# Performance work log

Hardware: AMD Instinct MI355X
Metric: run time of the kernel (lower is better)

The kernel has to match this reference:

```python
import jax, jax.numpy as jnp
import numpy as np

H, L, D, R = 16, 4096, 64, 128   # heads, seq len, head dim, FAVOR+ feature dim
S_SCALE = 0.125                  # attention inner-product scaling S
CHUNK = 128                      # chunk size for causal linear attention
EPS = 1e-10                      # module's self.epsilon denominator guard


def _get_proj(d, r, seed=0):
    # get_proj(R, D, orthogonal=True, hyperbolic=True): QR-orthogonalized
    # Gaussian block rescaled by chi column norms, then [W, -W].
    rng = np.random.RandomState(seed)
    rh = r // 2
    w = rng.randn(d, rh)
    chis = np.linalg.norm(w, ord=2, axis=0, keepdims=True)
    qm, _ = np.linalg.qr(w, mode='reduced')
    w = qm * chis
    return np.concatenate((w, -w), axis=1).astype(np.float32)  # (D, R)


def setup_inputs() -> dict:
    key = jax.random.key(0)
    kq, kk, kv = jax.random.split(key, 3)
    q = jax.random.normal(kq, (H, L, D), dtype=jnp.float32)
    k = jax.random.normal(kk, (H, L, D), dtype=jnp.float32)
    v = jax.random.normal(kv, (H, L, D), dtype=jnp.float32)
    W = jnp.asarray(_get_proj(D, R))
    return {"T": 64, "k": k, "q": q, "v": v, "W": W}


def _phi(x, W):
    # FAVOR+ feature map: x' = x * S^0.5 / D^0.25;
    # phi(x) = exp(W^T x' - ||x'||^2 / 2) / sqrt(R)
    xs = x * (S_SCALE ** 0.5 / D ** 0.25)            # (H, L, D)
    Wx = jnp.einsum('hld,dr->hlr', xs, W)            # (H, L, R)
    sq = 0.5 * jnp.sum(xs * xs, axis=-1, keepdims=True)
    return jnp.exp(Wx - sq) / (R ** 0.5)             # (H, L, R)


def reference(T, k, q, v, W):
    # Deterministic FAVOR+ estimator of the strictly-causal softmax attention
    # Pred_l = sum_{j<l} v_j exp(S<q_l,k_j>) / sum_{i<l} exp(S<q_l,k_i>)
    # which the tree+sampling machinery approximates (T = sampling budget,
    # irrelevant for the exact kernel estimate). Chunked linear attention.
    del T
    pq = _phi(q, W)                                  # (H, L, R)
    pk = _phi(k, W)                                  # (H, L, R)
    nc = L // CHUNK
    pq_c = pq.reshape(H, nc, CHUNK, R)
    pk_c = pk.reshape(H, nc, CHUNK, R)
    v_c = v.reshape(H, nc, CHUNK, D)
    # per-chunk KV summaries and exclusive prefix over chunks
    skv = jnp.einsum('hncr,hncd->hnrd', pk_c, v_c)   # (H, nc, R, D)
    zk = jnp.sum(pk_c, axis=2)                       # (H, nc, R)
    skv_prev = jnp.cumsum(skv, axis=1) - skv         # exclusive
    zk_prev = jnp.cumsum(zk, axis=1) - zk
    num_inter = jnp.einsum('hncr,hnrd->hncd', pq_c, skv_prev)
    den_inter = jnp.einsum('hncr,hnr->hnc', pq_c, zk_prev)
    # intra-chunk strictly-causal part (j < l)
    A = jnp.einsum('hncr,hnsr->hncs', pq_c, pk_c)    # (H, nc, C, C)
    mask = jnp.tril(jnp.ones((CHUNK, CHUNK), dtype=A.dtype), k=-1)
    A = A * mask
    num_intra = jnp.einsum('hncs,hnsd->hncd', A, v_c)
    den_intra = jnp.sum(A, axis=-1)
    out = (num_inter + num_intra) / (den_inter + den_intra + EPS)[..., None]
    return out.reshape(H, L, D)
```

## Files before the change

### kernel.cpp

```cpp
#include <hip/hip_runtime.h>

#define H 16
#define L 4096
#define D 64
#define R 128
#define C2 64
#define NC2 64
#define HN2 (H * NC2)
#define EPS 1e-10f
#define XS_SCALE 0.125f
#define PHI_SCALE 0.08838834764831845f

typedef __attribute__((ext_vector_type(8))) short bf8;
typedef __attribute__((ext_vector_type(4))) short bf4;
typedef __attribute__((ext_vector_type(16))) float facc16;

static __device__ __forceinline__ unsigned short f2b(float f) {
    unsigned u = __float_as_uint(f);
    return (unsigned short)((u + 0x7fffu + ((u >> 16) & 1u)) >> 16);
}
static __device__ __forceinline__ float b2f(unsigned short s) {
    return __uint_as_float(((unsigned)s) << 16);
}

__global__ __launch_bounds__(256) void kW(const float* __restrict__ W,
                                          unsigned short* __restrict__ Wtg) {
    for (int i = threadIdx.x; i < 8192; i += 256) {
        int d = i >> 7, r = i & 127;
        Wtg[(unsigned)((r * 64 + d) ^ ((r & 7) << 3))] = f2b(W[i]);
    }
}

__global__ __launch_bounds__(256, 4) void k1(
    const float* __restrict__ q, const float* __restrict__ k,
    const float* __restrict__ v, const unsigned short* __restrict__ Wtg,
    unsigned short* __restrict__ pq, unsigned short* __restrict__ pk,
    unsigned short* __restrict__ vTg, unsigned short* __restrict__ skvTp,
    float* __restrict__ zk)
{
    __shared__ __align__(16) unsigned short A_[8192];
    __shared__ __align__(16) unsigned short B_[4096];
    __shared__ __align__(16) unsigned short C_[8192];
    const int tid = threadIdx.x, hn = blockIdx.x;
    const int lane = tid & 63, wave = tid >> 6, lo = lane & 31, hi = lane >> 5;
    const int rg = wave & 1, ch = wave >> 1;
    const size_t cbase = (size_t)hn * C2 * D;
    const int prow = tid >> 4, pd0 = (tid & 15) * 4;

    float4 kv4[4];
    #pragma unroll
    for (int n = 0; n < 4; ++n)
        kv4[n] = *(const float4*)(k + cbase + (prow + 16 * n) * 64 + pd0);
    for (int i = tid; i < 1024; i += 256)
        *(bf8*)&A_[i * 8] = *(const bf8*)(Wtg + i * 8);
    #pragma unroll
    for (int n = 0; n < 4; ++n) {
        int row = prow + 16 * n;
        float4 vv = *(const float4*)(q + cbase + row * 64 + pd0);
        unsigned* p = (unsigned*)&B_[(unsigned)((row * 64 + pd0) ^ ((row & 7) << 3))];
        p[0] = (unsigned)f2b(vv.x * XS_SCALE) | ((unsigned)f2b(vv.y * XS_SCALE) << 16);
        p[1] = (unsigned)f2b(vv.z * XS_SCALE) | ((unsigned)f2b(vv.w * XS_SCALE) << 16);
    }
    __syncthreads();

    {
        bf8 af[4]; float ssq = 0.f;
        #pragma unroll
        for (int s = 0; s < 4; ++s) {
            af[s] = *(const bf8*)&B_[(unsigned)(((rg * 32 + lo) * 64 + 16 * s + 8 * hi) ^ ((lo & 7) << 3))];
            #pragma unroll
            for (int e = 0; e < 8; ++e) { float t = b2f((unsigned short)af[s][e]); ssq += t * t; }
        }
        ssq += __shfl_xor(ssq, 32); ssq *= 0.5f;
        float sqrow[16];
        #pragma unroll
        for (int reg = 0; reg < 16; ++reg)
            sqrow[reg] = __shfl(ssq, (reg & 3) + 8 * (reg >> 2) + 4 * hi);
        facc16 acc[2];
        #pragma unroll
        for (int t = 0; t < 2; ++t)
            #pragma unroll
            for (int e = 0; e < 16; ++e) acc[t][e] = 0.f;
        #pragma unroll
        for (int s = 0; s < 4; ++s)
            #pragma unroll
            for (int t = 0; t < 2; ++t) {
                const bf8 b = *(const bf8*)&A_[(unsigned)((((2 * ch + t) * 32 + lo) * 64 + 16 * s + 8 * hi) ^ ((lo & 7) << 3))];
                acc[t] = __builtin_amdgcn_mfma_f32_32x32x16_bf16(af[s], b, acc[t], 0, 0, 0);
            }
        #pragma unroll
        for (int t = 0; t < 2; ++t)
            #pragma unroll
            for (int reg = 0; reg < 16; ++reg) {
                int row = rg * 32 + (reg & 3) + 8 * (reg >> 2) + 4 * hi;
                int col = (2 * ch + t) * 32 + lo;
                C_[(unsigned)((row * 128 + col) ^ ((row & 15) << 3))] =
                    f2b(__expf(acc[t][reg] - sqrow[reg]) * PHI_SCALE);
            }
    }
    __syncthreads();

    float4 vv4[4];
    #pragma unroll
    for (int n = 0; n < 4; ++n)
        vv4[n] = *(const float4*)(v + cbase + (prow + 16 * n) * 64 + pd0);
    for (int i = tid; i < 1024; i += 256)
        *(bf8*)(pq + (size_t)hn * 8192 + i * 8) = *(const bf8*)&C_[i * 8];
    #pragma unroll
    for (int n = 0; n < 4; ++n) {
        int row = prow + 16 * n;
        unsigned* p = (unsigned*)&B_[(unsigned)((row * 64 + pd0) ^ ((row & 7) << 3))];
        p[0] = (unsigned)f2b(kv4[n].x * XS_SCALE) | ((unsigned)f2b(kv4[n].y * XS_SCALE) << 16);
        p[1] = (unsigned)f2b(kv4[n].z * XS_SCALE) | ((unsigned)f2b(kv4[n].w * XS_SCALE) << 16);
    }
    __syncthreads();

    facc16 acck[2];
    float sqk[16];
    {
        bf8 af[4]; float ssq = 0.f;
        #pragma unroll
        for (int s = 0; s < 4; ++s) {
            af[s] = *(const bf8*)&B_[(unsigned)(((rg * 32 + lo) * 64 + 16 * s + 8 * hi) ^ ((lo & 7) << 3))];
            #pragma unroll
            for (int e = 0; e < 8; ++e) { float t = b2f((unsigned short)af[s][e]); ssq += t * t; }
        }
        ssq += __shfl_xor(ssq, 32); ssq *= 0.5f;
        #pragma unroll
        for (int reg = 0; reg < 16; ++reg)
            sqk[reg] = __shfl(ssq, (reg & 3) + 8 * (reg >> 2) + 4 * hi);
        #pragma unroll
        for (int t = 0; t < 2; ++t)
            #pragma unroll
            for (int e = 0; e < 16; ++e) acck[t][e] = 0.f;
        #pragma unroll
        for (int s = 0; s < 4; ++s)
            #pragma unroll
            for (int t = 0; t < 2; ++t) {
                const bf8 b = *(const bf8*)&A_[(unsigned)((((2 * ch + t) * 32 + lo) * 64 + 16 * s + 8 * hi) ^ ((lo & 7) << 3))];
                acck[t] = __builtin_amdgcn_mfma_f32_32x32x16_bf16(af[s], b, acck[t], 0, 0, 0);
            }
    }
    __syncthreads();

    #pragma unroll
    for (int t = 0; t < 2; ++t) {
        int colr = (2 * ch + t) * 32 + lo;
        #pragma unroll
        for (int g = 0; g < 4; ++g) {
            int c0 = rg * 32 + 8 * g + 4 * hi;
            bf4 pk4;
            #pragma unroll
            for (int e = 0; e < 4; ++e) {
                unsigned short b = f2b(__expf(acck[t][4 * g + e] - sqk[4 * g + e]) * PHI_SCALE);
                pk4[e] = (short)b;
                C_[(unsigned)(((c0 + e) * 128 + colr) ^ (((c0 + e) & 15) << 3))] = b;
            }
            *(bf4*)&A_[(unsigned)((colr * 64 + c0) ^ ((colr & 7) << 3))] = pk4;
        }
    }
    #pragma unroll
    for (int n = 0; n < 4; ++n) {
        int row = prow + 16 * n;
        unsigned* p = (unsigned*)&B_[(unsigned)((row * 64 + pd0) ^ ((row & 7) << 3))];
        p[0] = (unsigned)f2b(vv4[n].x) | ((unsigned)f2b(vv4[n].y) << 16);
        p[1] = (unsigned)f2b(vv4[n].z) | ((unsigned)f2b(vv4[n].w) << 16);
    }
    __syncthreads();

    for (int i = tid; i < 1024; i += 256)
        *(bf8*)(pk + (size_t)hn * 8192 + i * 8) = *(const bf8*)&C_[i * 8];
    if (tid < 128) {
        float s = 0.f;
        #pragma unroll
        for (int j = 0; j < 8; ++j) {
            bf8 a8 = *(const bf8*)&A_[(unsigned)((tid * 64 + 8 * j) ^ ((tid & 7) << 3))];
            #pragma unroll
            for (int e = 0; e < 8; ++e) s += b2f((unsigned short)a8[e]);
        }
        zk[(size_t)hn * 128 + tid] = s;
    }
    bf8 aid[2];
    #pragma unroll
    for (int s2 = 0; s2 < 2; ++s2)
        #pragma unroll
        for (int e = 0; e < 8; ++e)
            aid[s2][e] = (e == lo - 16 * s2 - 8 * hi) ? (short)0x3F80 : (short)0;
    facc16 tv[2][2];
    #pragma unroll
    for (int t = 0; t < 2; ++t)
        #pragma unroll
        for (int u = 0; u < 2; ++u) {
            #pragma unroll
            for (int e = 0; e < 16; ++e) tv[t][u][e] = 0.f;
            #pragma unroll
            for (int s2 = 0; s2 < 2; ++s2) {
                const bf8 b = *(const bf8*)&B_[(unsigned)(((32 * u + lo) * 64 + 16 * (2 * t + s2) + 8 * hi) ^ ((lo & 7) << 3))];
                tv[t][u] = __builtin_amdgcn_mfma_f32_32x32x16_bf16(aid[s2], b, tv[t][u], 0, 0, 0);
            }
        }
    __syncthreads();

    #pragma unroll
    for (int t = 0; t < 2; ++t)
        #pragma unroll
        for (int u = 0; u < 2; ++u)
            #pragma unroll
            for (int reg = 0; reg < 16; ++reg) {
                int d = 32 * t + (reg & 3) + 8 * (reg >> 2) + 4 * hi;
                int c = 32 * u + lo;
                C_[(unsigned)((d * 64 + c) ^ ((d & 7) << 3))] = f2b(tv[t][u][reg]);
            }
    __syncthreads();

    for (int i = tid; i < 512; i += 256)
        *(bf8*)(vTg + (size_t)hn * 4096 + i * 8) = *(const bf8*)&C_[i * 8];
    {
        facc16 acs[2];
        #pragma unroll
        for (int t = 0; t < 2; ++t)
            #pragma unroll
            for (int e = 0; e < 16; ++e) acs[t][e] = 0.f;
        #pragma unroll
        for (int s = 0; s < 4; ++s) {
            const bf8 a = *(const bf8*)&C_[(unsigned)(((rg * 32 + lo) * 64 + 16 * s + 8 * hi) ^ ((lo & 7) << 3))];
            #pragma unroll
            for (int t = 0; t < 2; ++t) {
                const bf8 b = *(const bf8*)&A_[(unsigned)((((2 * ch + t) * 32 + lo) * 64 + 16 * s + 8 * hi) ^ ((lo & 7) << 3))];
                acs[t] = __builtin_amdgcn_mfma_f32_32x32x16_bf16(a, b, acs[t], 0, 0, 0);
            }
        }
        unsigned short* sg = skvTp + (size_t)hn * 8192;
        #pragma unroll
        for (int t = 0; t < 2; ++t)
            #pragma unroll
            for (int reg = 0; reg < 16; ++reg) {
                int d = rg * 32 + (reg & 3) + 8 * (reg >> 2) + 4 * hi;
                int r = (2 * ch + t) * 32 + lo;
                sg[d * 128 + r] = f2b(acs[t][reg]);
            }
    }
}

__global__ __launch_bounds__(256) void k2(unsigned short* __restrict__ skvTp,
                                          const float* __restrict__ zk,
                                          unsigned short* __restrict__ zkp)
{
    const int bid = blockIdx.x, tid = threadIdx.x;
    if (bid < 512) {
        int g = bid * 256 + tid;
        int h = g >> 13, dr = g & 8191;
        unsigned short* p = skvTp + (size_t)h * NC2 * 8192 + dr;
        unsigned short vals[NC2];
        #pragma unroll
        for (int n = 0; n < NC2; ++n) vals[n] = p[(size_t)n * 8192];
        float run = 0.f;
        #pragma unroll
        for (int n = 0; n < NC2; ++n) {
            float t = b2f(vals[n]);
            p[(size_t)n * 8192] = f2b(run);
            run += t;
        }
    } else {
        int g2 = (bid - 512) * 256 + tid;
        int h = g2 >> 7, r = g2 & 127;
        const float* pz = zk + (size_t)h * NC2 * 128 + r;
        unsigned short* oz = zkp + (size_t)h * NC2 * 128 + r;
        float vals[NC2];
        #pragma unroll
        for (int n = 0; n < NC2; ++n) vals[n] = pz[n * 128];
        float run = 0.f;
        #pragma unroll
        for (int n = 0; n < NC2; ++n) {
            oz[n * 128] = f2b(run);
            run += vals[n];
        }
    }
}

__global__ __launch_bounds__(256) void k3(
    const unsigned short* __restrict__ pq, const unsigned short* __restrict__ pk,
    const unsigned short* __restrict__ vTg, const unsigned short* __restrict__ skvTp,
    const unsigned short* __restrict__ zkp, float* __restrict__ out)
{
    __shared__ __align__(16) unsigned short P_[8192];
    __shared__ __align__(16) unsigned short Q_[8192];
    __shared__ __align__(16) unsigned short V_[4096];
    const int tid = threadIdx.x, hn = blockIdx.x;
    const int lane = tid & 63, wave = tid >> 6, lo = lane & 31, hi = lane >> 5;
    const int rg = wave & 1, ch = wave >> 1;

    for (int i = tid; i < 1024; i += 256)
        *(bf8*)&P_[i * 8] = *(const bf8*)(pq + (size_t)hn * 8192 + i * 8);
    for (int i = tid; i < 1024; i += 256)
        *(bf8*)&Q_[i * 8] = *(const bf8*)(pk + (size_t)hn * 8192 + i * 8);
    for (int i = tid; i < 512; i += 256)
        *(bf8*)&V_[i * 8] = *(const bf8*)(vTg + (size_t)hn * 4096 + i * 8);
    __syncthreads();

    bf8 qf[8];
    #pragma unroll
    for (int s = 0; s < 8; ++s)
        qf[s] = *(const bf8*)&P_[(unsigned)(((rg * 32 + lo) * 128 + 16 * s + 8 * hi) ^ ((lo & 15) << 3))];
    __syncthreads();

    for (int i = tid; i < 1024; i += 256) {
        bf8 t8 = *(const bf8*)(skvTp + (size_t)hn * 8192 + i * 8);
        int d = i >> 4, r0 = (i & 15) * 8;
        *(bf8*)&P_[(unsigned)((d * 128 + r0) ^ ((d & 15) << 3))] = t8;
    }
    bf8 onesf, zf[8];
    #pragma unroll
    for (int e = 0; e < 8; ++e) onesf[e] = (lo == 0) ? (short)0x3F80 : (short)0;
    #pragma unroll
    for (int s = 0; s < 8; ++s)
        #pragma unroll
        for (int e = 0; e < 8; ++e) zf[s][e] = 0;
    if (lo == 0) {
        #pragma unroll
        for (int s = 0; s < 8; ++s)
            zf[s] = *(const bf8*)(zkp + (size_t)hn * 128 + 16 * s + 8 * hi);
    }

    facc16 ac1;
    #pragma unroll
    for (int e = 0; e < 16; ++e) ac1[e] = 0.f;
    #pragma unroll
    for (int s = 0; s < 8; ++s) {
        const bf8 b = *(const bf8*)&Q_[(unsigned)(((ch * 32 + lo) * 128 + 16 * s + 8 * hi) ^ ((lo & 15) << 3))];
        ac1 = __builtin_amdgcn_mfma_f32_32x32x16_bf16(qf[s], b, ac1, 0, 0, 0);
    }
    __syncthreads();

    #pragma unroll
    for (int reg = 0; reg < 16; ++reg) {
        int row = rg * 32 + (reg & 3) + 8 * (reg >> 2) + 4 * hi;
        int sc = ch * 32 + lo;
        Q_[(unsigned)((row * 64 + sc) ^ ((row & 7) << 3))] = f2b(sc < row ? ac1[reg] : 0.f);
    }
    __syncthreads();

    facc16 an, ad;
    #pragma unroll
    for (int e = 0; e < 16; ++e) { an[e] = 0.f; ad[e] = 0.f; }
    #pragma unroll
    for (int s = 0; s < 4; ++s) {
        const bf8 a = *(const bf8*)&Q_[(unsigned)(((rg * 32 + lo) * 64 + 16 * s + 8 * hi) ^ ((lo & 7) << 3))];
        const bf8 b = *(const bf8*)&V_[(unsigned)(((ch * 32 + lo) * 64 + 16 * s + 8 * hi) ^ ((lo & 7) << 3))];
        an = __builtin_amdgcn_mfma_f32_32x32x16_bf16(a, b, an, 0, 0, 0);
        ad = __builtin_amdgcn_mfma_f32_32x32x16_bf16(a, onesf, ad, 0, 0, 0);
    }
    #pragma unroll
    for (int s = 0; s < 8; ++s) {
        const bf8 b = *(const bf8*)&P_[(unsigned)(((ch * 32 + lo) * 128 + 16 * s + 8 * hi) ^ ((lo & 15) << 3))];
        an = __builtin_amdgcn_mfma_f32_32x32x16_bf16(qf[s], b, an, 0, 0, 0);
        ad = __builtin_amdgcn_mfma_f32_32x32x16_bf16(qf[s], zf[s], ad, 0, 0, 0);
    }
    float* og = out + (size_t)hn * C2 * D;
    #pragma unroll
    for (int reg = 0; reg < 16; ++reg) {
        int row = rg * 32 + (reg & 3) + 8 * (reg >> 2) + 4 * hi;
        float dv = __shfl(ad[reg], lane & 32);
        og[row * 64 + ch * 32 + lo] = an[reg] / (dv + EPS);
    }
}

extern "C" void kernel_launch(void* const* d_in, const int* in_sizes, int n_in,
                              void* d_out, int out_size, void* d_ws, size_t ws_size,
                              hipStream_t stream) {
    const float* k = (const float*)d_in[1];
    const float* q = (const float*)d_in[2];
    const float* v = (const float*)d_in[3];
    const float* W = (const float*)d_in[4];
    float* out = (float*)d_out;

    unsigned short* pq    = (unsigned short*)d_ws;
    unsigned short* pk    = pq + (size_t)HN2 * 8192;
    unsigned short* vTg   = pk + (size_t)HN2 * 8192;
    unsigned short* skvTp = vTg + (size_t)HN2 * 4096;
    unsigned short* Wtg   = skvTp + (size_t)HN2 * 8192;
    unsigned short* zkp   = Wtg + 8192;
    float* zk             = (float*)(zkp + (size_t)HN2 * 128);

    kW<<<1, 256, 0, stream>>>(W, Wtg);
    k1<<<HN2, 256, 0, stream>>>(q, k, v, Wtg, pq, pk, vTg, skvTp, zk);
    k2<<<520, 256, 0, stream>>>(skvTp, zk, zkp);
    k3<<<HN2, 256, 0, stream>>>(pq, pk, vTg, skvTp, zkp, out);
}
```

Measured before the change: 63.44 us.

## Store intermediates in MFMA fragment order and load operands directly from global

Stores W, phi(q), phi(k) and v^T in global memory already laid out as per-lane MFMA fragments. The consumer kernels can then load operands straight from global memory instead of staging them through LDS with barriers. k1 now reads q and k directly into registers and computes the squared norm in fp32. The zk column sum becomes an MFMA against a ones vector, and f2b switches to the HIP bf16 intrinsic. This cuts LDS traffic and barriers, and frees LDS in k3 for occupancy, at the cost of more scattered global loads that lean on the cache.

```diff
diff --git a/kernel.cpp b/kernel.cpp
--- a/kernel.cpp
+++ b/kernel.cpp
@@ -1,4 +1,5 @@
 #include <hip/hip_runtime.h>
+#include <hip/hip_bf16.h>
 
 #define H 16
 #define L 4096
@@ -16,26 +17,33 @@
 typedef __attribute__((ext_vector_type(16))) float facc16;
 
 static __device__ __forceinline__ unsigned short f2b(float f) {
-    unsigned u = __float_as_uint(f);
-    return (unsigned short)((u + 0x7fffu + ((u >> 16) & 1u)) >> 16);
+    union { __hip_bfloat16 h; unsigned short u; } c;
+    c.h = __float2bfloat16(f);
+    return c.u;
 }
 static __device__ __forceinline__ float b2f(unsigned short s) {
     return __uint_as_float(((unsigned)s) << 16);
 }
 
 __global__ __launch_bounds__(256) void kW(const float* __restrict__ W,
-                                          unsigned short* __restrict__ Wtg) {
-    for (int i = threadIdx.x; i < 8192; i += 256) {
-        int d = i >> 7, r = i & 127;
-        Wtg[(unsigned)((r * 64 + d) ^ ((r & 7) << 3))] = f2b(W[i]);
+                                          unsigned short* __restrict__ WF) {
+    __shared__ float wl[8192];
+    for (int i = threadIdx.x; i < 8192; i += 256) wl[i] = W[i];
+    __syncthreads();
+    for (int i = threadIdx.x; i < 1024; i += 256) {
+        int tile = i >> 8, s = (i >> 6) & 3, hi = (i >> 5) & 1, lo = i & 31;
+        int r = tile * 32 + lo;
+        #pragma unroll
+        for (int e = 0; e < 8; ++e)
+            WF[i * 8 + e] = f2b(wl[(16 * s + 8 * hi + e) * 128 + r]);
     }
 }
 
 __global__ __launch_bounds__(256, 4) void k1(
     const float* __restrict__ q, const float* __restrict__ k,
-    const float* __restrict__ v, const unsigned short* __restrict__ Wtg,
-    unsigned short* __restrict__ pq, unsigned short* __restrict__ pk,
-    unsigned short* __restrict__ vTg, unsigned short* __restrict__ skvTp,
+    const float* __restrict__ v, const unsigned short* __restrict__ WF,
+    unsigned short* __restrict__ pqF, unsigned short* __restrict__ pkF,
+    unsigned short* __restrict__ vTF, unsigned short* __restrict__ skvTp,
     float* __restrict__ zk)
 {
     __shared__ __align__(16) unsigned short A_[8192];
@@ -47,35 +55,29 @@
     const size_t cbase = (size_t)hn * C2 * D;
     const int prow = tid >> 4, pd0 = (tid & 15) * 4;
 
-    float4 kv4[4];
-    #pragma unroll
-    for (int n = 0; n < 4; ++n)
-        kv4[n] = *(const float4*)(k + cbase + (prow + 16 * n) * 64 + pd0);
-    for (int i = tid; i < 1024; i += 256)
-        *(bf8*)&A_[i * 8] = *(const bf8*)(Wtg + i * 8);
-    #pragma unroll
-    for (int n = 0; n < 4; ++n) {
-        int row = prow + 16 * n;
-        float4 vv = *(const float4*)(q + cbase + row * 64 + pd0);
-        unsigned* p = (unsigned*)&B_[(unsigned)((row * 64 + pd0) ^ ((row & 7) << 3))];
-        p[0] = (unsigned)f2b(vv.x * XS_SCALE) | ((unsigned)f2b(vv.y * XS_SCALE) << 16);
-        p[1] = (unsigned)f2b(vv.z * XS_SCALE) | ((unsigned)f2b(vv.w * XS_SCALE) << 16);
-    }
-    __syncthreads();
-
-    {
-        bf8 af[4]; float ssq = 0.f;
+    bf8 af[4];
+    float sqrow[16];
+    {
+        float ssq = 0.f;
         #pragma unroll
         for (int s = 0; s < 4; ++s) {
-            af[s] = *(const bf8*)&B_[(unsigned)(((rg * 32 + lo) * 64 + 16 * s + 8 * hi) ^ ((lo & 7) << 3))];
-            #pragma unroll
-            for (int e = 0; e < 8; ++e) { float t = b2f((unsigned short)af[s][e]); ssq += t * t; }
+            const float* qp = q + cbase + (rg * 32 + lo) * 64 + 16 * s + 8 * hi;
+            float4 f0 = *(const float4*)qp;
+            float4 f1 = *(const float4*)(qp + 4);
+            float x0 = f0.x * XS_SCALE, x1 = f0.y * XS_SCALE, x2 = f0.z * XS_SCALE, x3 = f0.w * XS_SCALE;
+            float x4 = f1.x * XS_SCALE, x5 = f1.y * XS_SCALE, x6 = f1.z * XS_SCALE, x7 = f1.w * XS_SCALE;
+            ssq += x0*x0 + x1*x1 + x2*x2 + x3*x3 + x4*x4 + x5*x5 + x6*x6 + x7*x7;
+            bf8 a;
+            a[0]=(short)f2b(x0); a[1]=(short)f2b(x1); a[2]=(short)f2b(x2); a[3]=(short)f2b(x3);
+            a[4]=(short)f2b(x4); a[5]=(short)f2b(x5); a[6]=(short)f2b(x6); a[7]=(short)f2b(x7);
+            af[s] = a;
         }
         ssq += __shfl_xor(ssq, 32); ssq *= 0.5f;
-        float sqrow[16];
-        #pragma unroll
-        for (int reg = 0; reg < 16; ++reg)
-            sqrow[reg] = __shfl(ssq, (reg & 3) + 8 * (reg >> 2) + 4 * hi);
+        #pragma unroll
+        for (int r2 = 0; r2 < 16; ++r2)
+            sqrow[r2] = __shfl(ssq, (r2 & 3) + 8 * (r2 >> 2) + 4 * hi);
+    }
+    {
         facc16 acc[2];
         #pragma unroll
         for (int t = 0; t < 2; ++t)
@@ -85,7 +87,7 @@
         for (int s = 0; s < 4; ++s)
             #pragma unroll
             for (int t = 0; t < 2; ++t) {
-                const bf8 b = *(const bf8*)&A_[(unsigned)((((2 * ch + t) * 32 + lo) * 64 + 16 * s + 8 * hi) ^ ((lo & 7) << 3))];
+                const bf8 b = *(const bf8*)(WF + (((2 * ch + t) * 4 + s) * 64 + hi * 32 + lo) * 8);
                 acc[t] = __builtin_amdgcn_mfma_f32_32x32x16_bf16(af[s], b, acc[t], 0, 0, 0);
             }
         #pragma unroll
@@ -100,47 +102,48 @@
     }
     __syncthreads();
 
-    float4 vv4[4];
-    #pragma unroll
-    for (int n = 0; n < 4; ++n)
-        vv4[n] = *(const float4*)(v + cbase + (prow + 16 * n) * 64 + pd0);
-    for (int i = tid; i < 1024; i += 256)
-        *(bf8*)(pq + (size_t)hn * 8192 + i * 8) = *(const bf8*)&C_[i * 8];
-    #pragma unroll
-    for (int n = 0; n < 4; ++n) {
-        int row = prow + 16 * n;
-        unsigned* p = (unsigned*)&B_[(unsigned)((row * 64 + pd0) ^ ((row & 7) << 3))];
-        p[0] = (unsigned)f2b(kv4[n].x * XS_SCALE) | ((unsigned)f2b(kv4[n].y * XS_SCALE) << 16);
-        p[1] = (unsigned)f2b(kv4[n].z * XS_SCALE) | ((unsigned)f2b(kv4[n].w * XS_SCALE) << 16);
-    }
-    __syncthreads();
-
+    {
+        int g2 = wave & 1, sh = wave >> 1;
+        #pragma unroll
+        for (int s2 = 0; s2 < 4; ++s2) {
+            int s = sh * 4 + s2;
+            bf8 t8 = *(const bf8*)&C_[(unsigned)(((g2 * 32 + lo) * 128 + 16 * s + 8 * hi) ^ ((lo & 15) << 3))];
+            *(bf8*)(pqF + (size_t)hn * 8192 + (size_t)(((g2 * 8 + s) * 64 + hi * 32 + lo) * 8)) = t8;
+        }
+    }
+    float sqk[16];
+    {
+        float ssq = 0.f;
+        #pragma unroll
+        for (int s = 0; s < 4; ++s) {
+            const float* kp = k + cbase + (rg * 32 + lo) * 64 + 16 * s + 8 * hi;
+            float4 f0 = *(const float4*)kp;
+            float4 f1 = *(const float4*)(kp + 4);
+            float x0 = f0.x * XS_SCALE, x1 = f0.y * XS_SCALE, x2 = f0.z * XS_SCALE, x3 = f0.w * XS_SCALE;
+            float x4 = f1.x * XS_SCALE, x5 = f1.y * XS_SCALE, x6 = f1.z * XS_SCALE, x7 = f1.w * XS_SCALE;
+            ssq += x0*x0 + x1*x1 + x2*x2 + x3*x3 + x4*x4 + x5*x5 + x6*x6 + x7*x7;
+            bf8 a;
+            a[0]=(short)f2b(x0); a[1]=(short)f2b(x1); a[2]=(short)f2b(x2); a[3]=(short)f2b(x3);
+            a[4]=(short)f2b(x4); a[5]=(short)f2b(x5); a[6]=(short)f2b(x6); a[7]=(short)f2b(x7);
+            af[s] = a;
+        }
+        ssq += __shfl_xor(ssq, 32); ssq *= 0.5f;
+        #pragma unroll
+        for (int r2 = 0; r2 < 16; ++r2)
+            sqk[r2] = __shfl(ssq, (r2 & 3) + 8 * (r2 >> 2) + 4 * hi);
+    }
     facc16 acck[2];
-    float sqk[16];
-    {
-        bf8 af[4]; float ssq = 0.f;
-        #pragma unroll
-        for (int s = 0; s < 4; ++s) {
-            af[s] = *(const bf8*)&B_[(unsigned)(((rg * 32 + lo) * 64 + 16 * s + 8 * hi) ^ ((lo & 7) << 3))];
-            #pragma unroll
-            for (int e = 0; e < 8; ++e) { float t = b2f((unsigned short)af[s][e]); ssq += t * t; }
-        }
-        ssq += __shfl_xor(ssq, 32); ssq *= 0.5f;
-        #pragma unroll
-        for (int reg = 0; reg < 16; ++reg)
-            sqk[reg] = __shfl(ssq, (reg & 3) + 8 * (reg >> 2) + 4 * hi);
-        #pragma unroll
-        for (int t = 0; t < 2; ++t)
-            #pragma unroll
-            for (int e = 0; e < 16; ++e) acck[t][e] = 0.f;
-        #pragma unroll
-        for (int s = 0; s < 4; ++s)
-            #pragma unroll
-            for (int t = 0; t < 2; ++t) {
-                const bf8 b = *(const bf8*)&A_[(unsigned)((((2 * ch + t) * 32 + lo) * 64 + 16 * s + 8 * hi) ^ ((lo & 7) << 3))];
-                acck[t] = __builtin_amdgcn_mfma_f32_32x32x16_bf16(af[s], b, acck[t], 0, 0, 0);
-            }
-    }
+    #pragma unroll
+    for (int t = 0; t < 2; ++t)
+        #pragma unroll
+        for (int e = 0; e < 16; ++e) acck[t][e] = 0.f;
+    #pragma unroll
+    for (int s = 0; s < 4; ++s)
+        #pragma unroll
+        for (int t = 0; t < 2; ++t) {
+            const bf8 b = *(const bf8*)(WF + (((2 * ch + t) * 4 + s) * 64 + hi * 32 + lo) * 8);
+            acck[t] = __builtin_amdgcn_mfma_f32_32x32x16_bf16(af[s], b, acck[t], 0, 0, 0);
+        }
     __syncthreads();
 
     #pragma unroll
@@ -152,9 +155,9 @@
             bf4 pk4;
             #pragma unroll
             for (int e = 0; e < 4; ++e) {
-                unsigned short b = f2b(__expf(acck[t][4 * g + e] - sqk[4 * g + e]) * PHI_SCALE);
-                pk4[e] = (short)b;
-                C_[(unsigned)(((c0 + e) * 128 + colr) ^ (((c0 + e) & 15) << 3))] = b;
+                unsigned short bb = f2b(__expf(acck[t][4 * g + e] - sqk[4 * g + e]) * PHI_SCALE);
+                pk4[e] = (short)bb;
+                C_[(unsigned)(((c0 + e) * 128 + colr) ^ (((c0 + e) & 15) << 3))] = bb;
             }
             *(bf4*)&A_[(unsigned)((colr * 64 + c0) ^ ((colr & 7) << 3))] = pk4;
         }
@@ -162,23 +165,39 @@
     #pragma unroll
     for (int n = 0; n < 4; ++n) {
         int row = prow + 16 * n;
+        float4 vv = *(const float4*)(v + cbase + row * 64 + pd0);
         unsigned* p = (unsigned*)&B_[(unsigned)((row * 64 + pd0) ^ ((row & 7) << 3))];
-        p[0] = (unsigned)f2b(vv4[n].x) | ((unsigned)f2b(vv4[n].y) << 16);
-        p[1] = (unsigned)f2b(vv4[n].z) | ((unsigned)f2b(vv4[n].w) << 16);
-    }
-    __syncthreads();
-
-    for (int i = tid; i < 1024; i += 256)
-        *(bf8*)(pk + (size_t)hn * 8192 + i * 8) = *(const bf8*)&C_[i * 8];
-    if (tid < 128) {
-        float s = 0.f;
-        #pragma unroll
-        for (int j = 0; j < 8; ++j) {
-            bf8 a8 = *(const bf8*)&A_[(unsigned)((tid * 64 + 8 * j) ^ ((tid & 7) << 3))];
-            #pragma unroll
-            for (int e = 0; e < 8; ++e) s += b2f((unsigned short)a8[e]);
-        }
-        zk[(size_t)hn * 128 + tid] = s;
+        p[0] = (unsigned)f2b(vv.x) | ((unsigned)f2b(vv.y) << 16);
+        p[1] = (unsigned)f2b(vv.z) | ((unsigned)f2b(vv.w) << 16);
+    }
+    __syncthreads();
+
+    {
+        int g2 = wave & 1, sh = wave >> 1;
+        #pragma unroll
+        for (int s2 = 0; s2 < 4; ++s2) {
+            int s = sh * 4 + s2;
+            bf8 t8 = *(const bf8*)&C_[(unsigned)(((g2 * 32 + lo) * 128 + 16 * s + 8 * hi) ^ ((lo & 15) << 3))];
+            *(bf8*)(pkF + (size_t)hn * 8192 + (size_t)(((g2 * 8 + s) * 64 + hi * 32 + lo) * 8)) = t8;
+        }
+    }
+    {
+        bf8 onesk;
+        #pragma unroll
+        for (int e = 0; e < 8; ++e) onesk[e] = (lo == 0) ? (short)0x3F80 : (short)0;
+        facc16 az;
+        #pragma unroll
+        for (int e = 0; e < 16; ++e) az[e] = 0.f;
+        #pragma unroll
+        for (int s = 0; s < 4; ++s) {
+            const bf8 a = *(const bf8*)&A_[(unsigned)(((wave * 32 + lo) * 64 + 16 * s + 8 * hi) ^ ((lo & 7) << 3))];
+            az = __builtin_amdgcn_mfma_f32_32x32x16_bf16(a, onesk, az, 0, 0, 0);
+        }
+        if (lo == 0) {
+            #pragma unroll
+            for (int reg = 0; reg < 16; ++reg)
+                zk[(size_t)hn * 128 + wave * 32 + (reg & 3) + 8 * (reg >> 2) + 4 * hi] = az[reg];
+        }
     }
     bf8 aid[2];
     #pragma unroll
@@ -213,8 +232,15 @@
             }
     __syncthreads();
 
-    for (int i = tid; i < 512; i += 256)
-        *(bf8*)(vTg + (size_t)hn * 4096 + i * 8) = *(const bf8*)&C_[i * 8];
+    {
+        int g2 = wave & 1, sh = wave >> 1;
+        #pragma unroll
+        for (int s2 = 0; s2 < 2; ++s2) {
+            int s = sh * 2 + s2;
+            bf8 t8 = *(const bf8*)&C_[(unsigned)(((g2 * 32 + lo) * 64 + 16 * s + 8 * hi) ^ ((lo & 7) << 3))];
+            *(bf8*)(vTF + (size_t)hn * 4096 + (size_t)(((g2 * 4 + s) * 64 + hi * 32 + lo) * 8)) = t8;
+        }
+    }
     {
         facc16 acs[2];
         #pragma unroll
@@ -279,36 +305,25 @@
 }
 
 __global__ __launch_bounds__(256) void k3(
-    const unsigned short* __restrict__ pq, const unsigned short* __restrict__ pk,
-    const unsigned short* __restrict__ vTg, const unsigned short* __restrict__ skvTp,
+    const unsigned short* __restrict__ pqF, const unsigned short* __restrict__ pkF,
+    const unsigned short* __restrict__ vTF, const unsigned short* __restrict__ skvTp,
     const unsigned short* __restrict__ zkp, float* __restrict__ out)
 {
     __shared__ __align__(16) unsigned short P_[8192];
-    __shared__ __align__(16) unsigned short Q_[8192];
-    __shared__ __align__(16) unsigned short V_[4096];
+    __shared__ __align__(16) unsigned short S_[4096];
     const int tid = threadIdx.x, hn = blockIdx.x;
     const int lane = tid & 63, wave = tid >> 6, lo = lane & 31, hi = lane >> 5;
     const int rg = wave & 1, ch = wave >> 1;
 
-    for (int i = tid; i < 1024; i += 256)
-        *(bf8*)&P_[i * 8] = *(const bf8*)(pq + (size_t)hn * 8192 + i * 8);
-    for (int i = tid; i < 1024; i += 256)
-        *(bf8*)&Q_[i * 8] = *(const bf8*)(pk + (size_t)hn * 8192 + i * 8);
-    for (int i = tid; i < 512; i += 256)
-        *(bf8*)&V_[i * 8] = *(const bf8*)(vTg + (size_t)hn * 4096 + i * 8);
-    __syncthreads();
-
-    bf8 qf[8];
-    #pragma unroll
-    for (int s = 0; s < 8; ++s)
-        qf[s] = *(const bf8*)&P_[(unsigned)(((rg * 32 + lo) * 128 + 16 * s + 8 * hi) ^ ((lo & 15) << 3))];
-    __syncthreads();
-
     for (int i = tid; i < 1024; i += 256) {
-        bf8 t8 = *(const bf8*)(skvTp + (size_t)hn * 8192 + i * 8);
+        bf8 t8 = *(const bf8*)(skvTp + (size_t)hn * 8192 + (size_t)i * 8);
         int d = i >> 4, r0 = (i & 15) * 8;
         *(bf8*)&P_[(unsigned)((d * 128 + r0) ^ ((d & 15) << 3))] = t8;
     }
+    bf8 qf[8];
+    #pragma unroll
+    for (int s = 0; s < 8; ++s)
+        qf[s] = *(const bf8*)(pqF + (size_t)hn * 8192 + (size_t)(((rg * 8 + s) * 64 + hi * 32 + lo) * 8));
     bf8 onesf, zf[8];
     #pragma unroll
     for (int e = 0; e < 8; ++e) onesf[e] = (lo == 0) ? (short)0x3F80 : (short)0;
@@ -327,16 +342,14 @@
     for (int e = 0; e < 16; ++e) ac1[e] = 0.f;
     #pragma unroll
     for (int s = 0; s < 8; ++s) {
-        const bf8 b = *(const bf8*)&Q_[(unsigned)(((ch * 32 + lo) * 128 + 16 * s + 8 * hi) ^ ((lo & 15) << 3))];
+        const bf8 b = *(const bf8*)(pkF + (size_t)hn * 8192 + (size_t)(((ch * 8 + s) * 64 + hi * 32 + lo) * 8));
         ac1 = __builtin_amdgcn_mfma_f32_32x32x16_bf16(qf[s], b, ac1, 0, 0, 0);
     }
-    __syncthreads();
-
     #pragma unroll
     for (int reg = 0; reg < 16; ++reg) {
         int row = rg * 32 + (reg & 3) + 8 * (reg >> 2) + 4 * hi;
         int sc = ch * 32 + lo;
-        Q_[(unsigned)((row * 64 + sc) ^ ((row & 7) << 3))] = f2b(sc < row ? ac1[reg] : 0.f);
+        S_[(unsigned)((row * 64 + sc) ^ ((row & 7) << 3))] = f2b(sc < row ? ac1[reg] : 0.f);
     }
     __syncthreads();
 
@@ -345,8 +358,8 @@
     for (int e = 0; e < 16; ++e) { an[e] = 0.f; ad[e] = 0.f; }
     #pragma unroll
     for (int s = 0; s < 4; ++s) {
-        const bf8 a = *(const bf8*)&Q_[(unsigned)(((rg * 32 + lo) * 64 + 16 * s + 8 * hi) ^ ((lo & 7) << 3))];
-        const bf8 b = *(const bf8*)&V_[(unsigned)(((ch * 32 + lo) * 64 + 16 * s + 8 * hi) ^ ((lo & 7) << 3))];
+        const bf8 a = *(const bf8*)&S_[(unsigned)(((rg * 32 + lo) * 64 + 16 * s + 8 * hi) ^ ((lo & 7) << 3))];
+        const bf8 b = *(const bf8*)(vTF + (size_t)hn * 4096 + (size_t)(((ch * 4 + s) * 64 + hi * 32 + lo) * 8));
         an = __builtin_amdgcn_mfma_f32_32x32x16_bf16(a, b, an, 0, 0, 0);
         ad = __builtin_amdgcn_mfma_f32_32x32x16_bf16(a, onesf, ad, 0, 0, 0);
     }
@@ -374,16 +387,16 @@
     const float* W = (const float*)d_in[4];
     float* out = (float*)d_out;
 
-    unsigned short* pq    = (unsigned short*)d_ws;
-    unsigned short* pk    = pq + (size_t)HN2 * 8192;
-    unsigned short* vTg   = pk + (size_t)HN2 * 8192;
-    unsigned short* skvTp = vTg + (size_t)HN2 * 4096;
-    unsigned short* Wtg   = skvTp + (size_t)HN2 * 8192;
-    unsigned short* zkp   = Wtg + 8192;
+    unsigned short* pqF   = (unsigned short*)d_ws;
+    unsigned short* pkF   = pqF + (size_t)HN2 * 8192;
+    unsigned short* vTF   = pkF + (size_t)HN2 * 8192;
+    unsigned short* skvTp = vTF + (size_t)HN2 * 4096;
+    unsigned short* WF    = skvTp + (size_t)HN2 * 8192;
+    unsigned short* zkp   = WF + 8192;
     float* zk             = (float*)(zkp + (size_t)HN2 * 128);
 
-    kW<<<1, 256, 0, stream>>>(W, Wtg);
-    k1<<<HN2, 256, 0, stream>>>(q, k, v, Wtg, pq, pk, vTg, skvTp, zk);
+    kW<<<1, 256, 0, stream>>>(W, WF);
+    k1<<<HN2, 256, 0, stream>>>(q, k, v, WF, pqF, pkF, vTF, skvTp, zk);
     k2<<<520, 256, 0, stream>>>(skvTp, zk, zkp);
-    k3<<<HN2, 256, 0, stream>>>(pq, pk, vTg, skvTp, zkp, out);
-}
+    k3<<<HN2, 256, 0, stream>>>(pqF, pkF, vTF, skvTp, zkp, out);
+}
```

Result: faster. 54.79 us (-13.6%).
